# Performance work log

Hardware: AMD Instinct MI355X
Metric: run time of the kernel (lower is better)

## Reference

```python
import jax, jax.numpy as jnp
import numpy as np

N_NODES = 50000
N_EDGES = 800000
N_FEAT = 128
HIDDEN = 128
N_CLASSES = 10
N_GRAPHS = 100


def setup_inputs() -> dict:
    key = jax.random.key(0)
    ks = jax.random.split(key, 16)
    x = jax.random.normal(ks[0], (N_NODES, N_FEAT), dtype=jnp.float32)
    edge_index = jax.random.randint(ks[1], (2, N_EDGES), 0, N_NODES, dtype=jnp.int64)
    batch = jnp.sort(jax.random.randint(ks[2], (N_NODES,), 0, N_GRAPHS, dtype=jnp.int64))

    def glorot(k, fi, fo):
        s = jnp.sqrt(6.0 / (fi + fo)).astype(jnp.float32)
        return jax.random.uniform(k, (fi, fo), jnp.float32, -s, s)

    return {
        "x": x,
        "edge_index": edge_index,
        "batch": batch,
        "W1": glorot(ks[3], N_FEAT, HIDDEN),
        "b1": jnp.zeros((HIDDEN,), jnp.float32),
        "W2": glorot(ks[4], HIDDEN, HIDDEN),
        "b2": jnp.zeros((HIDDEN,), jnp.float32),
        "W3": glorot(ks[5], HIDDEN, HIDDEN // 2),
        "b3": jnp.zeros((HIDDEN // 2,), jnp.float32),
        "Wf1": glorot(ks[6], HIDDEN // 2, 32),
        "bf1": jnp.zeros((32,), jnp.float32),
        "Wf2": glorot(ks[7], 32, N_CLASSES),
        "bf2": jnp.zeros((N_CLASSES,), jnp.float32),
    }


def _gcn_conv(x, row, col, norm, W, b, n_nodes):
    # GCNConv: x' = D^{-1/2}(A+I)D^{-1/2} (x W) + b
    h = x @ W                                            # [N, out]
    msg = h[row] * norm[:, None]                         # gather + scale per edge
    out = jax.ops.segment_sum(msg, col, num_segments=n_nodes)  # scatter-add to targets
    return out + b


def reference(x, edge_index, batch, W1, b1, W2, b2, W3, b3, Wf1, bf1, Wf2, bf2):
    n = x.shape[0]
    # add self-loops (PyG GCNConv default)
    loop = jnp.arange(n, dtype=edge_index.dtype)
    row = jnp.concatenate([edge_index[0], loop])
    col = jnp.concatenate([edge_index[1], loop])
    # symmetric normalization from in-degree at targets (edge_weight = 1)
    deg = jax.ops.segment_sum(jnp.ones_like(col, x.dtype), col, num_segments=n)
    dinv = jnp.where(deg > 0, jax.lax.rsqrt(deg), 0.0)
    norm = dinv[row] * dinv[col]                         # [E + N]

    h = jax.nn.relu(_gcn_conv(x, row, col, norm, W1, b1, n))
    h = jax.nn.relu(_gcn_conv(h, row, col, norm, W2, b2, n))
    h = jax.nn.relu(_gcn_conv(h, row, col, norm, W3, b3, n))

    # global_mean_pool over graphs
    sums = jax.ops.segment_sum(h, batch, num_segments=N_GRAPHS)
    cnts = jax.ops.segment_sum(jnp.ones((n,), h.dtype), batch, num_segments=N_GRAPHS)
    pooled = sums / jnp.maximum(cnts, 1.0)[:, None]      # [G, hidden//2]

    h = jax.nn.relu(pooled @ Wf1 + bf1)
    logits = h @ Wf2 + bf2                               # [G, num_classes]
    return logits
```

## Files before the change

kernel.cpp:

```cpp
#include <hip/hip_runtime.h>
#include <hip/hip_fp16.h>


#define NGRAPH 100
#define CAP 64

typedef _Float16 f16x8 __attribute__((ext_vector_type(8)));
typedef float f32x4 __attribute__((ext_vector_type(4)));


__global__ __launch_bounds__(256) void prep_all(const float* __restrict__ W1,
                                                const float* __restrict__ W2,
                                                const float* __restrict__ W3,
                                                __half* __restrict__ Wt1,
                                                __half* __restrict__ Wt2,
                                                __half* __restrict__ Wt3,
                                                int* __restrict__ cnt,
                                                float* __restrict__ pooled, int n) {
    const int idx = blockIdx.x * 256 + threadIdx.x;
    if (idx < 16384) {
        int nn = idx >> 7, k = idx & 127;
        Wt1[idx] = __float2half(W1[k * 128 + nn]);
    } else if (idx < 32768) {
        int j = idx - 16384;
        int nn = j >> 7, k = j & 127;
        Wt2[j] = __float2half(W2[k * 128 + nn]);
    } else if (idx < 40960) {
        int j = idx - 32768;
        int nn = j >> 7, k = j & 127;
        Wt3[j] = __float2half(W3[k * 64 + nn]);
    }
    if (idx < n) cnt[idx] = 0;
    if (idx < NGRAPH * 64) pooled[idx] = 0.0f;
}


__global__ void fill_bucket(const int* __restrict__ row, const int* __restrict__ col,
                            int* __restrict__ cnt, int* __restrict__ bucket,
                            int E, int colsPerGroup) {
    const int g  = blockIdx.x & 7;
    const int gb = blockIdx.x >> 3;
    const int nb = gridDim.x >> 3;
    const int lo = g * colsPerGroup, hi = lo + colsPerGroup;
    for (int e = gb * 256 + threadIdx.x; e < E; e += nb * 256) {
        int c = col[e];
        if (c >= lo && c < hi) {
            int pos = atomicAdd(&cnt[c], 1);
            bucket[c * CAP + pos] = row[e];
        }
    }
}


template <int OUT, bool F16IN>
__global__ __launch_bounds__(256) void gemm_mfma(const void* __restrict__ Xv,
                                                 const __half* __restrict__ Wt,
                                                 const float* __restrict__ bias_in,
                                                 const int* __restrict__ cnt,
                                                 __half* __restrict__ Yh, int n) {
    __shared__ _Float16 Xs[64 * 128];
    __shared__ _Float16 Ws[OUT * 128];
    __shared__ float bs[128];

    const float*  Xf = (const float*)Xv;
    const __half* Xh = (const __half*)Xv;

    const int t = threadIdx.x;
    if (t < 128) bs[t] = (bias_in != nullptr) ? bias_in[t] : 0.0f;
    __syncthreads();

    const int row0 = blockIdx.x * 64;
    const bool do_relu = (bias_in != nullptr);

    for (int c = t; c < 64 * 16; c += 256) {
        const int r = c >> 4, q = c & 15;
        const int gr = row0 + r;
        float vals[8];
        #pragma unroll
        for (int i = 0; i < 8; ++i) vals[i] = 0.0f;
        if (gr < n) {
            if (F16IN) {
                f16x8 hv = *(const f16x8*)&Xh[(size_t)gr * 128 + q * 8];
                #pragma unroll
                for (int i = 0; i < 8; ++i) vals[i] = (float)hv[i];
            } else {
                float4 va = *(const float4*)&Xf[(size_t)gr * 128 + q * 8];
                float4 vb = *(const float4*)&Xf[(size_t)gr * 128 + q * 8 + 4];
                vals[0] = va.x; vals[1] = va.y; vals[2] = va.z; vals[3] = va.w;
                vals[4] = vb.x; vals[5] = vb.y; vals[6] = vb.z; vals[7] = vb.w;
            }
        }
        if (do_relu) {
            const int k = q * 8;
            #pragma unroll
            for (int i = 0; i < 8; ++i) vals[i] = fmaxf(vals[i] + bs[k + i], 0.f);
        }
        f16x8 hv;
        #pragma unroll
        for (int i = 0; i < 8; ++i) hv[i] = (_Float16)vals[i];
        *(f16x8*)&Xs[(size_t)((r << 4) + (q ^ (r & 15))) * 8] = hv;
    }
    for (int c = t; c < OUT * 16; c += 256) {
        const int nn = c >> 4, q = c & 15;
        f16x8 w = *(const f16x8*)&Wt[nn * 128 + q * 8];
        *(f16x8*)&Ws[(size_t)((nn << 4) + (q ^ (nn & 15))) * 8] = w;
    }
    __syncthreads();

    constexpr int NT = OUT / 16;
    const int lane = t & 63, wave = t >> 6;
    const int m = lane & 15, quad = lane >> 4;

    f32x4 acc[NT];
    #pragma unroll
    for (int i = 0; i < NT; ++i) acc[i] = (f32x4){0.f, 0.f, 0.f, 0.f};

    #pragma unroll
    for (int s = 0; s < 4; ++s) {
        const int qa = s * 4 + quad;
        f16x8 a = *(const f16x8*)&Xs[(size_t)(((wave * 16 + m) << 4) + (qa ^ m)) * 8];
        #pragma unroll
        for (int tt = 0; tt < NT; ++tt) {
            f16x8 b = *(const f16x8*)&Ws[(size_t)(((tt * 16 + m) << 4) + (qa ^ m)) * 8];
            acc[tt] = __builtin_amdgcn_mfma_f32_16x16x32_f16(a, b, acc[tt], 0, 0, 0);
        }
    }

    #pragma unroll
    for (int i = 0; i < 4; ++i) {
        const int gr = row0 + wave * 16 + quad * 4 + i;
        if (gr < n) {
            const float dw = 1.0f / sqrtf((float)(cnt[gr] + 1));
            #pragma unroll
            for (int tt = 0; tt < NT; ++tt)
                Yh[(size_t)gr * OUT + tt * 16 + m] = __float2half(acc[tt][i] * dw);
        }
    }
}


template <int F>
__global__ void gather_kernel(const __half* __restrict__ hs, const int* __restrict__ cnt,
                              const int* __restrict__ bucket,
                              __half* __restrict__ outh, int n) {
    const int lane = threadIdx.x & 63;
    const int c = (blockIdx.x * blockDim.x + threadIdx.x) >> 6;
    if (c >= n) return;
    const int beg = c * CAP;
    const int end = beg + cnt[c];
    const float w = 1.0f / sqrtf((float)(cnt[c] + 1));
    const float2* hq = (const float2*)hs;

    auto cvt = [](float2 raw) {
        __half2 ha = *(__half2*)&raw.x;
        __half2 hb = *(__half2*)&raw.y;
        float2 fa = __half22float2(ha);
        float2 fb = __half22float2(hb);
        return make_float4(fa.x, fa.y, fb.x, fb.y);
    };
    auto pack = [](float4 v) {
        float2 o;
        *(__half2*)&o.x = __float22half2_rn(make_float2(v.x, v.y));
        *(__half2*)&o.y = __float22half2_rn(make_float2(v.z, v.w));
        return o;
    };

    if (F == 128) {
        const int half = lane >> 5;
        const int l    = lane & 31;
        float4 acc = make_float4(0.f, 0.f, 0.f, 0.f);
        if (half == 0) acc = cvt(hq[(size_t)c * 32 + l]);
        int j = beg + half;
        for (; j + 6 < end; j += 8) {
            int s0 = bucket[j], s1 = bucket[j + 2], s2 = bucket[j + 4], s3 = bucket[j + 6];
            float4 v0 = cvt(hq[(size_t)s0 * 32 + l]);
            float4 v1 = cvt(hq[(size_t)s1 * 32 + l]);
            float4 v2 = cvt(hq[(size_t)s2 * 32 + l]);
            float4 v3 = cvt(hq[(size_t)s3 * 32 + l]);
            acc.x += v0.x + v1.x + v2.x + v3.x;
            acc.y += v0.y + v1.y + v2.y + v3.y;
            acc.z += v0.z + v1.z + v2.z + v3.z;
            acc.w += v0.w + v1.w + v2.w + v3.w;
        }
        for (; j < end; j += 2) {
            float4 v = cvt(hq[(size_t)bucket[j] * 32 + l]);
            acc.x += v.x; acc.y += v.y; acc.z += v.z; acc.w += v.w;
        }
        acc.x += __shfl(acc.x, lane ^ 32);
        acc.y += __shfl(acc.y, lane ^ 32);
        acc.z += __shfl(acc.z, lane ^ 32);
        acc.w += __shfl(acc.w, lane ^ 32);
        if (half == 0) {
            float4 o = make_float4(w * acc.x, w * acc.y, w * acc.z, w * acc.w);
            *(float2*)&outh[(size_t)c * 128 + l * 4] = pack(o);
        }
    } else {
        const int q = lane >> 4;
        const int l = lane & 15;
        float4 acc = make_float4(0.f, 0.f, 0.f, 0.f);
        if (q == 0) acc = cvt(hq[(size_t)c * 16 + l]);
        int j = beg + q;
        for (; j + 12 < end; j += 16) {
            int s0 = bucket[j], s1 = bucket[j + 4], s2 = bucket[j + 8], s3 = bucket[j + 12];
            float4 v0 = cvt(hq[(size_t)s0 * 16 + l]);
            float4 v1 = cvt(hq[(size_t)s1 * 16 + l]);
            float4 v2 = cvt(hq[(size_t)s2 * 16 + l]);
            float4 v3 = cvt(hq[(size_t)s3 * 16 + l]);
            acc.x += v0.x + v1.x + v2.x + v3.x;
            acc.y += v0.y + v1.y + v2.y + v3.y;
            acc.z += v0.z + v1.z + v2.z + v3.z;
            acc.w += v0.w + v1.w + v2.w + v3.w;
        }
        for (; j < end; j += 4) {
            float4 v = cvt(hq[(size_t)bucket[j] * 16 + l]);
            acc.x += v.x; acc.y += v.y; acc.z += v.z; acc.w += v.w;
        }
        acc.x += __shfl(acc.x, lane ^ 16);
        acc.y += __shfl(acc.y, lane ^ 16);
        acc.z += __shfl(acc.z, lane ^ 16);
        acc.w += __shfl(acc.w, lane ^ 16);
        acc.x += __shfl(acc.x, lane ^ 32);
        acc.y += __shfl(acc.y, lane ^ 32);
        acc.z += __shfl(acc.z, lane ^ 32);
        acc.w += __shfl(acc.w, lane ^ 32);
        if (q == 0) {
            float4 o = make_float4(w * acc.x, w * acc.y, w * acc.z, w * acc.w);
            *(float2*)&outh[(size_t)c * 64 + l * 4] = pack(o);
        }
    }
}


__global__ __launch_bounds__(256) void fused_gpool(const __half* __restrict__ hs,
                                                   const int* __restrict__ cnt,
                                                   const int* __restrict__ bucket,
                                                   const float* __restrict__ b3,
                                                   const int* __restrict__ batch,
                                                   float* __restrict__ pooled, int n) {
    const int lane  = threadIdx.x & 63;
    const int wave  = (blockIdx.x * blockDim.x + threadIdx.x) >> 6;
    const int nwav  = (gridDim.x * blockDim.x) >> 6;
    const int chunk = (n + nwav - 1) / nwav;
    const int beg = wave * chunk;
    const int end = min(beg + chunk, n);
    if (beg >= end) return;
    const float bias = b3[lane];
    int curg = batch[beg];
    float acc = 0.f;
    for (int i = beg; i < end; ++i) {
        int g = batch[i];
        if (g != curg) {
            atomicAdd(&pooled[curg * 64 + lane], acc);
            acc = 0.f; curg = g;
        }
        const int deg = cnt[i];
        const float dv = 1.0f / sqrtf((float)(deg + 1));
        float sv = __half2float(hs[(size_t)i * 64 + lane]);
        const int eb = i * CAP, ee = eb + deg;
        int j = eb;
        float s1 = 0.f;
        for (; j + 7 < ee; j += 8) {
            int a0 = bucket[j],     a1 = bucket[j + 1], a2 = bucket[j + 2], a3 = bucket[j + 3];
            int a4 = bucket[j + 4], a5 = bucket[j + 5], a6 = bucket[j + 6], a7 = bucket[j + 7];
            sv += __half2float(hs[(size_t)a0 * 64 + lane])
                + __half2float(hs[(size_t)a1 * 64 + lane])
                + __half2float(hs[(size_t)a2 * 64 + lane])
                + __half2float(hs[(size_t)a3 * 64 + lane]);
            s1 += __half2float(hs[(size_t)a4 * 64 + lane])
                + __half2float(hs[(size_t)a5 * 64 + lane])
                + __half2float(hs[(size_t)a6 * 64 + lane])
                + __half2float(hs[(size_t)a7 * 64 + lane]);
        }
        for (; j < ee; ++j) sv += __half2float(hs[(size_t)bucket[j] * 64 + lane]);
        sv += s1;
        acc += fmaxf(dv * sv + bias, 0.f);
    }
    atomicAdd(&pooled[curg * 64 + lane], acc);
}


__global__ __launch_bounds__(64) void mlp_kernel(const float* __restrict__ pooled,
                                                 const int* __restrict__ batch,
                                                 const float* __restrict__ Wf1,
                                                 const float* __restrict__ bf1,
                                                 const float* __restrict__ Wf2,
                                                 const float* __restrict__ bf2,
                                                 float* __restrict__ out, int n) {
    const int g = blockIdx.x;
    const int t = threadIdx.x;

    auto lb = [&](int v) {
        int lo = 0, hi = n;
        while (lo < hi) { int mid = (lo + hi) >> 1; if (batch[mid] < v) lo = mid + 1; else hi = mid; }
        return lo;
    };
    const int cnt = lb(g + 1) - lb(g);

    __shared__ float pm[64];
    __shared__ float hid[32];

    pm[t] = pooled[g * 64 + t] / (float)(cnt > 0 ? cnt : 1);
    __syncthreads();

    if (t < 32) {
        float a = bf1[t];
        #pragma unroll
        for (int k = 0; k < 64; ++k) a += pm[k] * Wf1[k * 32 + t];
        hid[t] = fmaxf(a, 0.f);
    }
    __syncthreads();

    if (t < 10) {
        float a = bf2[t];
        #pragma unroll
        for (int k = 0; k < 32; ++k) a += hid[k] * Wf2[k * 10 + t];
        out[g * 10 + t] = a;
    }
}


extern "C" void kernel_launch(void* const* d_in, const int* in_sizes, int n_in,
                              void* d_out, int out_size, void* d_ws, size_t ws_size,
                              hipStream_t stream) {
    const float* x     = (const float*)d_in[0];
    const int*   edge  = (const int*)  d_in[1];
    const int*   batch = (const int*)  d_in[2];
    const float* W1    = (const float*)d_in[3];
    const float* b1    = (const float*)d_in[4];
    const float* W2    = (const float*)d_in[5];
    const float* b2    = (const float*)d_in[6];
    const float* W3    = (const float*)d_in[7];
    const float* b3    = (const float*)d_in[8];
    const float* Wf1   = (const float*)d_in[9];
    const float* bf1   = (const float*)d_in[10];
    const float* Wf2   = (const float*)d_in[11];
    const float* bf2   = (const float*)d_in[12];
    float* out = (float*)d_out;

    const int E = in_sizes[1] / 2;
    const int n = in_sizes[2];
    const int* row = edge;
    const int* col = edge + E;

    const int colsPerGroup = (n + 7) / 8;

    const size_t n_pad = ((size_t)n + 64) & ~(size_t)63;
    char* wsb = (char*)d_ws;
    int*    cnt    = (int*)wsb;                  wsb += n_pad * 4;
    float*  pooled = (float*)wsb;                wsb += NGRAPH * 64 * 4;
    int*    bucket = (int*)wsb;                  wsb += (size_t)n_pad * CAP * 4;
    __half* Wt1    = (__half*)wsb;               wsb += 16384 * 2;
    __half* Wt2    = (__half*)wsb;               wsb += 16384 * 2;
    __half* Wt3    = (__half*)wsb;               wsb += 8192 * 2;
    __half* bufA   = (__half*)wsb;               wsb += (size_t)n * 128 * 2;
    __half* bufB   = (__half*)wsb;

    prep_all<<<256, 256, 0, stream>>>(W1, W2, W3, Wt1, Wt2, Wt3, cnt, pooled, n);
    fill_bucket<<<1024, 256, 0, stream>>>(row, col, cnt, bucket, E, colsPerGroup);

    const int ggemm = (n + 63) / 64;
    const int gath_grid = (n * 64 + 255) / 256;

    gemm_mfma<128, false><<<ggemm, 256, 0, stream>>>(x, Wt1, nullptr, cnt, bufA, n);
    gather_kernel<128><<<gath_grid, 256, 0, stream>>>(bufA, cnt, bucket, bufB, n);
    gemm_mfma<128, true><<<ggemm, 256, 0, stream>>>(bufB, Wt2, b1, cnt, bufA, n);
    gather_kernel<128><<<gath_grid, 256, 0, stream>>>(bufA, cnt, bucket, bufB, n);
    gemm_mfma<64, true><<<ggemm, 256, 0, stream>>>(bufB, Wt3, b2, cnt, bufA, n);
    fused_gpool<<<1536, 256, 0, stream>>>(bufA, cnt, bucket, b3, batch, pooled, n);
    mlp_kernel<<<NGRAPH, 64, 0, stream>>>(pooled, batch, Wf1, bf1, Wf2, bf2, out, n);
}
```

Baseline: 288.4 us.

## Fuse MLP head into pooling kernel via last-block flag and split neighbor lanes

The separate MLP kernel is folded into the final gather-pool kernel: each block bumps a global done counter, and the last block to finish computes the per-graph mean and the two dense layers with wave shuffles. The gather loop now reads half2 pairs, with the two 32-lane halves of each wave taking alternating neighbors and combining through a shuffle. The grid grows from 1536 to 2048 blocks. This removes one kernel launch and raises memory parallelism per node, but the final MLP runs serially in a single block.

```diff
diff --git a/kernel.cpp b/kernel.cpp
--- a/kernel.cpp
+++ b/kernel.cpp
@@ -16,7 +16,8 @@
                                                 __half* __restrict__ Wt2,
                                                 __half* __restrict__ Wt3,
                                                 int* __restrict__ cnt,
-                                                float* __restrict__ pooled, int n) {
+                                                float* __restrict__ pooled,
+                                                int* __restrict__ done, int n) {
     const int idx = blockIdx.x * 256 + threadIdx.x;
     if (idx < 16384) {
         int nn = idx >> 7, k = idx & 127;
@@ -32,6 +33,7 @@
     }
     if (idx < n) cnt[idx] = 0;
     if (idx < NGRAPH * 64) pooled[idx] = 0.0f;
+    if (idx == 0) *done = 0;
 }
 
 
@@ -236,85 +238,106 @@
                                                    const int* __restrict__ bucket,
                                                    const float* __restrict__ b3,
                                                    const int* __restrict__ batch,
-                                                   float* __restrict__ pooled, int n) {
+                                                   float* __restrict__ pooled,
+                                                   const float* __restrict__ Wf1,
+                                                   const float* __restrict__ bf1,
+                                                   const float* __restrict__ Wf2,
+                                                   const float* __restrict__ bf2,
+                                                   float* __restrict__ out,
+                                                   int* __restrict__ done, int n) {
     const int lane  = threadIdx.x & 63;
+    const int half  = lane >> 5;
+    const int li    = lane & 31;
     const int wave  = (blockIdx.x * blockDim.x + threadIdx.x) >> 6;
     const int nwav  = (gridDim.x * blockDim.x) >> 6;
     const int chunk = (n + nwav - 1) / nwav;
     const int beg = wave * chunk;
     const int end = min(beg + chunk, n);
-    if (beg >= end) return;
-    const float bias = b3[lane];
-    int curg = batch[beg];
-    float acc = 0.f;
-    for (int i = beg; i < end; ++i) {
-        int g = batch[i];
-        if (g != curg) {
-            atomicAdd(&pooled[curg * 64 + lane], acc);
-            acc = 0.f; curg = g;
-        }
-        const int deg = cnt[i];
-        const float dv = 1.0f / sqrtf((float)(deg + 1));
-        float sv = __half2float(hs[(size_t)i * 64 + lane]);
-        const int eb = i * CAP, ee = eb + deg;
-        int j = eb;
-        float s1 = 0.f;
-        for (; j + 7 < ee; j += 8) {
-            int a0 = bucket[j],     a1 = bucket[j + 1], a2 = bucket[j + 2], a3 = bucket[j + 3];
-            int a4 = bucket[j + 4], a5 = bucket[j + 5], a6 = bucket[j + 6], a7 = bucket[j + 7];
-            sv += __half2float(hs[(size_t)a0 * 64 + lane])
-                + __half2float(hs[(size_t)a1 * 64 + lane])
-                + __half2float(hs[(size_t)a2 * 64 + lane])
-                + __half2float(hs[(size_t)a3 * 64 + lane]);
-            s1 += __half2float(hs[(size_t)a4 * 64 + lane])
-                + __half2float(hs[(size_t)a5 * 64 + lane])
-                + __half2float(hs[(size_t)a6 * 64 + lane])
-                + __half2float(hs[(size_t)a7 * 64 + lane]);
-        }
-        for (; j < ee; ++j) sv += __half2float(hs[(size_t)bucket[j] * 64 + lane]);
-        sv += s1;
-        acc += fmaxf(dv * sv + bias, 0.f);
-    }
-    atomicAdd(&pooled[curg * 64 + lane], acc);
-}
-
-
-__global__ __launch_bounds__(64) void mlp_kernel(const float* __restrict__ pooled,
-                                                 const int* __restrict__ batch,
-                                                 const float* __restrict__ Wf1,
-                                                 const float* __restrict__ bf1,
-                                                 const float* __restrict__ Wf2,
-                                                 const float* __restrict__ bf2,
-                                                 float* __restrict__ out, int n) {
-    const int g = blockIdx.x;
-    const int t = threadIdx.x;
-
-    auto lb = [&](int v) {
+    const unsigned* h2 = (const unsigned*)hs;
+
+    auto cvt2 = [](unsigned raw) { return __half22float2(*(__half2*)&raw); };
+
+    if (beg < end) {
+        const float bias0 = b3[li * 2], bias1 = b3[li * 2 + 1];
+        int curg = batch[beg];
+        float2 acc = make_float2(0.f, 0.f);
+        for (int i = beg; i < end; ++i) {
+            int g = batch[i];
+            if (g != curg) {
+                if (half == 0) {
+                    atomicAdd(&pooled[curg * 64 + li * 2],     acc.x);
+                    atomicAdd(&pooled[curg * 64 + li * 2 + 1], acc.y);
+                }
+                acc = make_float2(0.f, 0.f); curg = g;
+            }
+            const int deg = cnt[i];
+            const float dv = 1.0f / sqrtf((float)(deg + 1));
+            float2 sv = make_float2(0.f, 0.f);
+            if (half == 0) sv = cvt2(h2[(size_t)i * 32 + li]);
+            const int eb = i * CAP, ee = eb + deg;
+            int j = eb + half;
+            for (; j + 14 < ee; j += 16) {
+                int a0 = bucket[j],      a1 = bucket[j + 2],  a2 = bucket[j + 4],  a3 = bucket[j + 6];
+                int a4 = bucket[j + 8],  a5 = bucket[j + 10], a6 = bucket[j + 12], a7 = bucket[j + 14];
+                float2 v0 = cvt2(h2[(size_t)a0 * 32 + li]);
+                float2 v1 = cvt2(h2[(size_t)a1 * 32 + li]);
+                float2 v2 = cvt2(h2[(size_t)a2 * 32 + li]);
+                float2 v3 = cvt2(h2[(size_t)a3 * 32 + li]);
+                float2 v4 = cvt2(h2[(size_t)a4 * 32 + li]);
+                float2 v5 = cvt2(h2[(size_t)a5 * 32 + li]);
+                float2 v6 = cvt2(h2[(size_t)a6 * 32 + li]);
+                float2 v7 = cvt2(h2[(size_t)a7 * 32 + li]);
+                sv.x += (v0.x + v1.x) + (v2.x + v3.x) + (v4.x + v5.x) + (v6.x + v7.x);
+                sv.y += (v0.y + v1.y) + (v2.y + v3.y) + (v4.y + v5.y) + (v6.y + v7.y);
+            }
+            for (; j < ee; j += 2) {
+                float2 v = cvt2(h2[(size_t)bucket[j] * 32 + li]);
+                sv.x += v.x; sv.y += v.y;
+            }
+            sv.x += __shfl(sv.x, lane ^ 32);
+            sv.y += __shfl(sv.y, lane ^ 32);
+            acc.x += fmaxf(dv * sv.x + bias0, 0.f);
+            acc.y += fmaxf(dv * sv.y + bias1, 0.f);
+        }
+        if (half == 0) {
+            atomicAdd(&pooled[curg * 64 + li * 2],     acc.x);
+            atomicAdd(&pooled[curg * 64 + li * 2 + 1], acc.y);
+        }
+    }
+
+    __shared__ int lastFlag;
+    __threadfence();
+    __syncthreads();
+    if (threadIdx.x == 0) {
+        int d = atomicAdd(done, 1);
+        lastFlag = (d == (int)gridDim.x - 1) ? 1 : 0;
+    }
+    __syncthreads();
+    if (!lastFlag) return;
+
+    const int w4 = threadIdx.x >> 6;
+    for (int g = w4 * 25; g < w4 * 25 + 25; ++g) {
         int lo = 0, hi = n;
-        while (lo < hi) { int mid = (lo + hi) >> 1; if (batch[mid] < v) lo = mid + 1; else hi = mid; }
-        return lo;
-    };
-    const int cnt = lb(g + 1) - lb(g);
-
-    __shared__ float pm[64];
-    __shared__ float hid[32];
-
-    pm[t] = pooled[g * 64 + t] / (float)(cnt > 0 ? cnt : 1);
-    __syncthreads();
-
-    if (t < 32) {
-        float a = bf1[t];
-        #pragma unroll
-        for (int k = 0; k < 64; ++k) a += pm[k] * Wf1[k * 32 + t];
-        hid[t] = fmaxf(a, 0.f);
-    }
-    __syncthreads();
-
-    if (t < 10) {
-        float a = bf2[t];
-        #pragma unroll
-        for (int k = 0; k < 32; ++k) a += hid[k] * Wf2[k * 10 + t];
-        out[g * 10 + t] = a;
+        while (lo < hi) { int mid = (lo + hi) >> 1; if (batch[mid] < g) lo = mid + 1; else hi = mid; }
+        const int s0 = lo;
+        lo = 0; hi = n;
+        while (lo < hi) { int mid = (lo + hi) >> 1; if (batch[mid] < g + 1) lo = mid + 1; else hi = mid; }
+        const int cg = lo - s0;
+        float pm = atomicAdd(&pooled[g * 64 + lane], 0.0f) / (float)(cg > 0 ? cg : 1);
+        float a = (lane < 32) ? bf1[lane] : 0.f;
+        #pragma unroll
+        for (int k = 0; k < 64; ++k) {
+            float pk = __shfl(pm, k);
+            if (lane < 32) a += pk * Wf1[k * 32 + lane];
+        }
+        float h = fmaxf(a, 0.f);
+        float o = (lane < 10) ? bf2[lane] : 0.f;
+        #pragma unroll
+        for (int k = 0; k < 32; ++k) {
+            float hk = __shfl(h, k);
+            if (lane < 10) o += hk * Wf2[k * 10 + lane];
+        }
+        if (lane < 10) out[g * 10 + lane] = o;
     }
 }
 
@@ -348,6 +371,7 @@
     char* wsb = (char*)d_ws;
     int*    cnt    = (int*)wsb;                  wsb += n_pad * 4;
     float*  pooled = (float*)wsb;                wsb += NGRAPH * 64 * 4;
+    int*    done   = (int*)wsb;                  wsb += 64 * 4;
     int*    bucket = (int*)wsb;                  wsb += (size_t)n_pad * CAP * 4;
     __half* Wt1    = (__half*)wsb;               wsb += 16384 * 2;
     __half* Wt2    = (__half*)wsb;               wsb += 16384 * 2;
@@ -355,7 +379,7 @@
     __half* bufA   = (__half*)wsb;               wsb += (size_t)n * 128 * 2;
     __half* bufB   = (__half*)wsb;
 
-    prep_all<<<256, 256, 0, stream>>>(W1, W2, W3, Wt1, Wt2, Wt3, cnt, pooled, n);
+    prep_all<<<256, 256, 0, stream>>>(W1, W2, W3, Wt1, Wt2, Wt3, cnt, pooled, done, n);
     fill_bucket<<<1024, 256, 0, stream>>>(row, col, cnt, bucket, E, colsPerGroup);
 
     const int ggemm = (n + 63) / 64;
@@ -366,6 +390,6 @@
     gemm_mfma<128, true><<<ggemm, 256, 0, stream>>>(bufB, Wt2, b1, cnt, bufA, n);
     gather_kernel<128><<<gath_grid, 256, 0, stream>>>(bufA, cnt, bucket, bufB, n);
     gemm_mfma<64, true><<<ggemm, 256, 0, stream>>>(bufB, Wt3, b2, cnt, bufA, n);
-    fused_gpool<<<1536, 256, 0, stream>>>(bufA, cnt, bucket, b3, batch, pooled, n);
-    mlp_kernel<<<NGRAPH, 64, 0, stream>>>(pooled, batch, Wf1, bf1, Wf2, bf2, out, n);
-}
+    fused_gpool<<<2048, 256, 0, stream>>>(bufA, cnt, bucket, b3, batch, pooled,
+                                          Wf1, bf1, Wf2, bf2, out, done, n);
+}
```

New measurement: 747.8 us. 159% more time.
